# Kernel tuning notes

Measured on AMD Instinct MI355X. Metric: run time of the kernel, lower is better.

## Reference

```python
import jax, jax.numpy as jnp
import numpy as np

N, B, C, K, FF = 1024, 8, 256, 4, 2048

def layer_norm(x, g, b, eps=1e-5):
    mu = jnp.mean(x, axis=-1, keepdims=True)
    var = jnp.var(x, axis=-1, keepdims=True)
    return (x - mu) / jnp.sqrt(var + eps) * g + b

def setup_inputs() -> dict:
    key = jax.random.key(0)
    ks = jax.random.split(key, 10)
    s = 0.02
    return {
        "src_tokens": jax.random.normal(ks[0], (N, B, C), jnp.float32),
        "matched_token_list": jax.random.normal(ks[1], (K, N, B, C), jnp.float32),
        "pos_embed": jax.random.normal(ks[2], (N, B, C), jnp.float32),
        "mask": jnp.zeros((B, N, N), jnp.float32),
        "W_agg": jax.random.normal(ks[3], (C * K, C), jnp.float32) * s,
        "b_agg": jnp.zeros((C,), jnp.float32),
        "W1": jax.random.normal(ks[4], (C, FF), jnp.float32) * s,
        "b1": jnp.zeros((FF,), jnp.float32),
        "W2": jax.random.normal(ks[5], (FF, C), jnp.float32) * s,
        "b2": jnp.zeros((C,), jnp.float32),
        "g1": jnp.ones((C,), jnp.float32),
        "be1": jnp.zeros((C,), jnp.float32),
        "g2": jnp.ones((C,), jnp.float32),
        "be2": jnp.zeros((C,), jnp.float32),
    }

def reference(src_tokens, matched_token_list, pos_embed, mask,
              W_agg, b_agg, W1, b1, W2, b2, g1, be1, g2, be2):
    # q: (n,b,c) -> (b,n,c); k/v: (K,n,b,c) -> (K,b,n,c)
    q = jnp.transpose(src_tokens + pos_embed, (1, 0, 2))
    k = jnp.transpose(matched_token_list + pos_embed[None], (0, 2, 1, 3))
    v = jnp.transpose(matched_token_list, (0, 2, 1, 3))
    q_scaled = q / jnp.sqrt(jnp.asarray(q.shape[-1], q.dtype))
    # scores: (K,b,n,n) with additive mask bias
    scores = jnp.einsum('bnc,kbmc->kbnm', q_scaled, k) + mask[None]
    attn = jax.nn.softmax(scores, axis=-1)
    out_k = jnp.einsum('kbnm,kbmc->kbnc', attn, v)  # (K,b,n,c)
    # concat over K on channel dim: (b,n,K*c)
    cat = jnp.transpose(out_k, (1, 2, 0, 3)).reshape(q.shape[0], q.shape[1], -1)
    rec = cat @ W_agg + b_agg  # (b,n,c)
    rec = jnp.transpose(rec, (1, 0, 2))  # (n,b,c)
    rec = layer_norm(src_tokens + rec, g1, be1)
    ffn = jax.nn.relu(rec @ W1 + b1) @ W2 + b2
    rec = layer_norm(rec + ffn, g2, be2)
    return rec
```

## Files before the change

### kernel.cpp

```cpp
#include <hip/hip_runtime.h>

#define N_SEQ 1024
#define B_SZ 8
#define C_DIM 256
#define K_HEADS 4
#define FF_DIM 2048

typedef short s16x8 __attribute__((ext_vector_type(8)));
typedef float f32x4v __attribute__((ext_vector_type(4)));

#define GLOAD_LDS16(src, dst)                                                              \
    __builtin_amdgcn_global_load_lds((const __attribute__((address_space(1))) void*)(src), \
                                     (__attribute__((address_space(3))) void*)(dst), 16, 0, 0)

__device__ __forceinline__ unsigned short f2bf(float f) {
    unsigned u = __builtin_bit_cast(unsigned, f);
    u += 0x7FFFu + ((u >> 16) & 1u);
    return (unsigned short)(u >> 16);
}


__global__ __launch_bounds__(256) void prep_q_kernel(const float* __restrict__ src,
                                                     const float* __restrict__ pos,
                                                     unsigned short* __restrict__ qb) {
    int t = blockIdx.x * 256 + threadIdx.x;
    int i4 = t * 4;
    float4 s = *reinterpret_cast<const float4*>(src + i4);
    float4 p = *reinterpret_cast<const float4*>(pos + i4);
    int n = i4 >> 11;
    int rem = i4 & 2047;
    int b = rem >> 8;
    int c = rem & 255;
    int out = (b * N_SEQ + n) * C_DIM + c;
    *reinterpret_cast<ushort4*>(qb + out) = make_ushort4(
        f2bf((s.x + p.x) * 0.0625f), f2bf((s.y + p.y) * 0.0625f),
        f2bf((s.z + p.z) * 0.0625f), f2bf((s.w + p.w) * 0.0625f));
}

__global__ __launch_bounds__(256) void prep_kv_kernel(const float* __restrict__ matched,
                                                      const float* __restrict__ pos,
                                                      unsigned short* __restrict__ kb,
                                                      unsigned short* __restrict__ vfrag) {
    __shared__ unsigned short Vl[64][256];
    int blk = blockIdx.x;
    int nt = blk & 15, pr = blk >> 4;
    int k = pr >> 3, b = pr & 7;
    int n0 = nt * 64;
    int t = threadIdx.x;
    int c4 = (t & 63) * 4;
#pragma unroll
    for (int r = 0; r < 16; r++) {
        int nl = (t >> 6) * 16 + r;
        int n = n0 + nl;
        size_t mi = ((size_t)(k * N_SEQ + n) * B_SZ + b) * C_DIM + c4;
        float4 m = *reinterpret_cast<const float4*>(matched + mi);
        float4 p = *reinterpret_cast<const float4*>(pos + ((size_t)n * B_SZ + b) * C_DIM + c4);
        *reinterpret_cast<ushort4*>(kb + ((size_t)pr * N_SEQ + n) * C_DIM + c4) =
            make_ushort4(f2bf(m.x + p.x), f2bf(m.y + p.y), f2bf(m.z + p.z), f2bf(m.w + p.w));
        *reinterpret_cast<ushort4*>(&Vl[nl][c4]) =
            make_ushort4(f2bf(m.x), f2bf(m.y), f2bf(m.z), f2bf(m.w));
    }
    __syncthreads();
#pragma unroll
    for (int h = 0; h < 2; h++) {
        unsigned short* tb = vfrag + ((size_t)(pr * 32 + nt * 2 + h)) * 8192;
#pragma unroll
        for (int g = 0; g < 4; g++) {
            int c2 = t + 256 * g;
            int ct = c2 >> 6;
            int lane2 = c2 & 63;
            int l152 = lane2 & 15, lg2 = lane2 >> 4;
            s16x8 v;
#pragma unroll
            for (int e = 0; e < 8; e++)
                v[e] = (short)Vl[h * 32 + lg2 * 8 + e][ct * 16 + l152];
            *reinterpret_cast<s16x8*>(tb + (size_t)c2 * 8) = v;
        }
    }
}

__global__ __launch_bounds__(256) void transpose_w_kernel(const float* __restrict__ W,
                                                          unsigned short* __restrict__ Wt,
                                                          int R, int Cn) {
    int idx = blockIdx.x * 256 + threadIdx.x;
    int c = idx / R;
    int r = idx - c * R;
    Wt[idx] = f2bf(W[(size_t)r * Cn + c]);
}

__global__ __launch_bounds__(256, 2) void attn_kernel(const unsigned short* __restrict__ qb,
                                                      const unsigned short* __restrict__ kb,
                                                      const unsigned short* __restrict__ vfrag,
                                                      const float* __restrict__ mask,
                                                      unsigned short* __restrict__ att) {
    __shared__ unsigned short Kl[2][8192];
    __shared__ unsigned short Psh[2][4][16][40];
    __shared__ float scl[2][4][17];
    __shared__ float lrex[4][17];

    int bx = blockIdx.x;
    int b = bx & 7;
    int r2 = bx >> 3;
    int kidx = r2 & 3;
    int qtb = r2 >> 2;
    int pr = kidx * 8 + b;

    int tid = threadIdx.x, wid = tid >> 6, lane = tid & 63;
    int l15 = lane & 15, lg = lane >> 4;
    int q0 = qtb * 64 + wid * 16;

    s16x8 qf[8];
    const unsigned short* qrow = qb + ((size_t)(b * N_SEQ + q0 + l15)) * C_DIM + lg * 8;
#pragma unroll
    for (int cc = 0; cc < 8; cc++) qf[cc] = *reinterpret_cast<const s16x8*>(qrow + cc * 32);

    f32x4v oacc[16];
#pragma unroll
    for (int i = 0; i < 16; i++) oacc[i] = (f32x4v){0.f, 0.f, 0.f, 0.f};
    float mrun = -3e38f, lrun = 0.f;

    const unsigned short* kbp = kb + (size_t)pr * N_SEQ * C_DIM;
    const unsigned short* vfp = vfrag + (size_t)pr * 32 * 8192 + lane * 8;
    const float* mrow = mask + ((size_t)b * N_SEQ + q0 + l15) * N_SEQ;

    auto stage_k = [&](int kv0, unsigned short* buf) {
#pragma unroll
        for (int i = 0; i < 4; i++) {
            int ch = (wid * 4 + i) * 64 + lane;
            int r = ch >> 5;
            int ce = ((ch & 31) * 8) ^ ((r & 7) << 3);
            GLOAD_LDS16(kbp + (size_t)(kv0 + r) * C_DIM + ce, &buf[(wid * 4 + i) * 512]);
        }
    };

    stage_k(0, &Kl[0][0]);
    f32x4v mc0 = *reinterpret_cast<const f32x4v*>(mrow + lg * 4);
    f32x4v mc1 = *reinterpret_cast<const f32x4v*>(mrow + 16 + lg * 4);

    int swz = (l15 & 7) << 3;
    for (int t = 0; t < 32; t++) {
        int cur = t & 1;
        int kv0 = t * 32;
        __syncthreads();
        if (t + 1 < 32) stage_k(kv0 + 32, &Kl[cur ^ 1][0]);

        const unsigned short* vsrc = vfp + (size_t)t * 8192;
        s16x8 vreg[4];
#pragma unroll
        for (int c = 0; c < 4; c++)
            vreg[c] = *reinterpret_cast<const s16x8*>(vsrc + (wid * 4 + c) * 512);

        f32x4v s0 = {0.f, 0.f, 0.f, 0.f}, s1 = {0.f, 0.f, 0.f, 0.f};
        const unsigned short* KlB = &Kl[cur][0];
        __builtin_amdgcn_s_setprio(1);
#pragma unroll
        for (int cc = 0; cc < 8; cc++) {
            s16x8 k0 = *reinterpret_cast<const s16x8*>(KlB + l15 * 256 + ((cc * 32 + lg * 8) ^ swz));
            s16x8 k1 = *reinterpret_cast<const s16x8*>(KlB + (16 + l15) * 256 + ((cc * 32 + lg * 8) ^ swz));
            s0 = __builtin_amdgcn_mfma_f32_16x16x32_bf16(k0, qf[cc], s0, 0, 0, 0);
            s1 = __builtin_amdgcn_mfma_f32_16x16x32_bf16(k1, qf[cc], s1, 0, 0, 0);
        }
        __builtin_amdgcn_s_setprio(0);
#pragma unroll
        for (int jj = 0; jj < 4; jj++) { s0[jj] += mc0[jj]; s1[jj] += mc1[jj]; }
        if (t + 1 < 32) {
            mc0 = *reinterpret_cast<const f32x4v*>(mrow + kv0 + 32 + lg * 4);
            mc1 = *reinterpret_cast<const f32x4v*>(mrow + kv0 + 48 + lg * 4);
        }

        float pm = fmaxf(fmaxf(fmaxf(s0[0], s0[1]), fmaxf(s0[2], s0[3])),
                         fmaxf(fmaxf(s1[0], s1[1]), fmaxf(s1[2], s1[3])));
        pm = fmaxf(pm, __shfl_xor(pm, 16));
        pm = fmaxf(pm, __shfl_xor(pm, 32));
        float sc = 1.0f;
        if (__any(pm > mrun + 8.f)) {
            float mn = fmaxf(mrun, pm);
            sc = __expf(mrun - mn);
            mrun = mn;
        }
        float p0[4], p1[4];
#pragma unroll
        for (int jj = 0; jj < 4; jj++) {
            p0[jj] = __expf(s0[jj] - mrun);
            p1[jj] = __expf(s1[jj] - mrun);
        }
        float ps = (p0[0] + p0[1]) + (p0[2] + p0[3]) + (p1[0] + p1[1]) + (p1[2] + p1[3]);
        ps += __shfl_xor(ps, 16);
        ps += __shfl_xor(ps, 32);
        lrun = lrun * sc + ps;

        *reinterpret_cast<ushort4*>(&Psh[cur][wid][l15][lg * 4]) =
            make_ushort4(f2bf(p0[0]), f2bf(p0[1]), f2bf(p0[2]), f2bf(p0[3]));
        *reinterpret_cast<ushort4*>(&Psh[cur][wid][l15][16 + lg * 4]) =
            make_ushort4(f2bf(p1[0]), f2bf(p1[1]), f2bf(p1[2]), f2bf(p1[3]));
        if (lane < 16) scl[cur][wid][lane] = sc;
        __syncthreads();

        __builtin_amdgcn_s_setprio(1);
#pragma unroll
        for (int j = 0; j < 4; j++) {
            float scj = scl[cur][j][l15];
            s16x8 pf = *reinterpret_cast<const s16x8*>(&Psh[cur][j][l15][lg * 8]);
#pragma unroll
            for (int c = 0; c < 4; c++) {
                int idx = j * 4 + c;
#pragma unroll
                for (int jj = 0; jj < 4; jj++) oacc[idx][jj] *= scj;
                oacc[idx] = __builtin_amdgcn_mfma_f32_16x16x32_bf16(vreg[c], pf, oacc[idx], 0, 0, 0);
            }
        }
        __builtin_amdgcn_s_setprio(0);
    }

    if (lane < 16) lrex[wid][lane] = lrun;
    __syncthreads();
#pragma unroll
    for (int j = 0; j < 4; j++) {
        float invj = 1.0f / lrex[j][l15];
#pragma unroll
        for (int c = 0; c < 4; c++) {
            int idx = j * 4 + c;
            size_t orow = ((size_t)(b * N_SEQ + qtb * 64 + j * 16 + l15)) * (K_HEADS * C_DIM)
                          + kidx * C_DIM + wid * 64 + c * 16 + lg * 4;
            *reinterpret_cast<ushort4*>(att + orow) =
                make_ushort4(f2bf(oacc[idx][0] * invj), f2bf(oacc[idx][1] * invj),
                             f2bf(oacc[idx][2] * invj), f2bf(oacc[idx][3] * invj));
        }
    }
}

template <int BM, int BN, int RELU, int OUTBF>
__global__ __launch_bounds__(256) void gemm_bt_kernel(const unsigned short* __restrict__ A,
                                                      const unsigned short* __restrict__ Bt,
                                                      const float* __restrict__ bias,
                                                      float* __restrict__ Cf,
                                                      unsigned short* __restrict__ Cb,
                                                      int M, int Nn, int Kd) {
    constexpr int WAVES_N = (BM == 128) ? 2 : 4;
    constexpr int WN = BN / WAVES_N;
    constexpr int NT = WN / 16;
    constexpr int TILE = (BM + BN) * 64;
    constexpr int CALLS = (BM + BN) / 32;
    __shared__ unsigned short Sl[2][TILE];
    int tm0 = blockIdx.y * BM, tn0 = blockIdx.x * BN;
    int tid = threadIdx.x, wid = tid >> 6, lane = tid & 63;
    int l15 = lane & 15, lg = lane >> 4;
    int wm = (wid / WAVES_N) * 64, wn = (wid % WAVES_N) * WN;

    f32x4v acc[4][NT];
#pragma unroll
    for (int i = 0; i < 4; i++)
#pragma unroll
        for (int j = 0; j < NT; j++) acc[i][j] = (f32x4v){0.f, 0.f, 0.f, 0.f};

    auto stage = [&](int k0, unsigned short* buf) {
#pragma unroll
        for (int i = 0; i < CALLS; i++) {
            int chb = (i * 4 + wid) * 64;
            int ch = chb + lane;
            const unsigned short* src;
            if (chb < BM * 8) {
                int r = ch >> 3;
                int c8 = ((ch & 7) * 8) ^ ((r & 7) << 3);
                src = A + (size_t)(tm0 + r) * Kd + k0 + c8;
            } else {
                int ch2 = ch - BM * 8;
                int r = ch2 >> 3;
                int c8 = ((ch2 & 7) * 8) ^ ((r & 7) << 3);
                src = Bt + (size_t)(tn0 + r) * Kd + k0 + c8;
            }
            GLOAD_LDS16(src, buf + chb * 8);
        }
    };

    stage(0, &Sl[0][0]);
    int nk = Kd >> 6;
    int swz = (l15 & 7) << 3;
    for (int kt = 0; kt < nk; kt++) {
        int cur = kt & 1;
        __syncthreads();
        if (kt + 1 < nk) stage((kt + 1) * 64, &Sl[cur ^ 1][0]);
        const unsigned short* SA = &Sl[cur][0];
        const unsigned short* SB = SA + BM * 64;
        s16x8 af[4][2], bf[NT][2];
#pragma unroll
        for (int mt = 0; mt < 4; mt++)
#pragma unroll
            for (int h = 0; h < 2; h++)
                af[mt][h] = *reinterpret_cast<const s16x8*>(
                    SA + (wm + mt * 16 + l15) * 64 + ((h * 32 + lg * 8) ^ swz));
#pragma unroll
        for (int nt = 0; nt < NT; nt++)
#pragma unroll
            for (int h = 0; h < 2; h++)
                bf[nt][h] = *reinterpret_cast<const s16x8*>(
                    SB + (wn + nt * 16 + l15) * 64 + ((h * 32 + lg * 8) ^ swz));
        __builtin_amdgcn_s_setprio(1);
#pragma unroll
        for (int mt = 0; mt < 4; mt++)
#pragma unroll
            for (int nt = 0; nt < NT; nt++) {
                acc[mt][nt] = __builtin_amdgcn_mfma_f32_16x16x32_bf16(af[mt][0], bf[nt][0], acc[mt][nt], 0, 0, 0);
                acc[mt][nt] = __builtin_amdgcn_mfma_f32_16x16x32_bf16(af[mt][1], bf[nt][1], acc[mt][nt], 0, 0, 0);
            }
        __builtin_amdgcn_s_setprio(0);
    }

#pragma unroll
    for (int mt = 0; mt < 4; mt++) {
#pragma unroll
        for (int nt = 0; nt < NT; nt++) {
#pragma unroll
            for (int j = 0; j < 4; j++) {
                int row = tm0 + wm + mt * 16 + lg * 4 + j;
                int col = tn0 + wn + nt * 16 + l15;
                float v = acc[mt][nt][j] + bias[col];
                if (RELU) v = fmaxf(v, 0.f);
                if (OUTBF) Cb[(size_t)row * Nn + col] = f2bf(v);
                else       Cf[(size_t)row * Nn + col] = v;
            }
        }
    }
}

__global__ __launch_bounds__(256) void ln1_kernel(const float* __restrict__ src,
                                                  const float* __restrict__ recT,
                                                  const float* __restrict__ g,
                                                  const float* __restrict__ be,
                                                  float* __restrict__ outf,
                                                  unsigned short* __restrict__ outb) {
    int r = blockIdx.x * 4 + (threadIdx.x >> 6);
    int lane = threadIdx.x & 63;
    int n = r >> 3, b = r & 7;
    int c = lane * 4;
    float4 xs = *reinterpret_cast<const float4*>(src + (size_t)r * C_DIM + c);
    float4 xr = *reinterpret_cast<const float4*>(recT + ((size_t)(b * N_SEQ + n)) * C_DIM + c);
    float x[4] = {xs.x + xr.x, xs.y + xr.y, xs.z + xr.z, xs.w + xr.w};
    float s = x[0] + x[1] + x[2] + x[3];
    float q = x[0] * x[0] + x[1] * x[1] + x[2] * x[2] + x[3] * x[3];
#pragma unroll
    for (int d = 1; d < 64; d <<= 1) {
        s += __shfl_xor(s, d);
        q += __shfl_xor(q, d);
    }
    float mean = s * (1.f / 256.f);
    float var = q * (1.f / 256.f) - mean * mean;
    float rstd = rsqrtf(var + 1e-5f);
    float4 gv = *reinterpret_cast<const float4*>(g + c);
    float4 bv = *reinterpret_cast<const float4*>(be + c);
    float y0 = (x[0] - mean) * rstd * gv.x + bv.x;
    float y1 = (x[1] - mean) * rstd * gv.y + bv.y;
    float y2 = (x[2] - mean) * rstd * gv.z + bv.z;
    float y3 = (x[3] - mean) * rstd * gv.w + bv.w;
    *reinterpret_cast<float4*>(outf + (size_t)r * C_DIM + c) = make_float4(y0, y1, y2, y3);
    *reinterpret_cast<ushort4*>(outb + (size_t)r * C_DIM + c) =
        make_ushort4(f2bf(y0), f2bf(y1), f2bf(y2), f2bf(y3));
}

__global__ __launch_bounds__(256) void ln2_kernel(const float* __restrict__ rec1f,
                                                  const float* __restrict__ ffn,
                                                  const float* __restrict__ g,
                                                  const float* __restrict__ be,
                                                  float* __restrict__ out) {
    int r = blockIdx.x * 4 + (threadIdx.x >> 6);
    int lane = threadIdx.x & 63;
    int c = lane * 4;
    size_t base = (size_t)r * C_DIM + c;
    float4 xa = *reinterpret_cast<const float4*>(rec1f + base);
    float4 xb = *reinterpret_cast<const float4*>(ffn + base);
    float x[4] = {xa.x + xb.x, xa.y + xb.y, xa.z + xb.z, xa.w + xb.w};
    float s = x[0] + x[1] + x[2] + x[3];
    float q = x[0] * x[0] + x[1] * x[1] + x[2] * x[2] + x[3] * x[3];
#pragma unroll
    for (int d = 1; d < 64; d <<= 1) {
        s += __shfl_xor(s, d);
        q += __shfl_xor(q, d);
    }
    float mean = s * (1.f / 256.f);
    float var = q * (1.f / 256.f) - mean * mean;
    float rstd = rsqrtf(var + 1e-5f);
    float4 gv = *reinterpret_cast<const float4*>(g + c);
    float4 bv = *reinterpret_cast<const float4*>(be + c);
    *reinterpret_cast<float4*>(out + base) = make_float4(
        (x[0] - mean) * rstd * gv.x + bv.x,
        (x[1] - mean) * rstd * gv.y + bv.y,
        (x[2] - mean) * rstd * gv.z + bv.z,
        (x[3] - mean) * rstd * gv.w + bv.w);
}


extern "C" void kernel_launch(void* const* d_in, const int* in_sizes, int n_in,
                              void* d_out, int out_size, void* d_ws, size_t ws_size,
                              hipStream_t stream) {
    const float* src   = (const float*)d_in[0];
    const float* match = (const float*)d_in[1];
    const float* pos   = (const float*)d_in[2];
    const float* mask  = (const float*)d_in[3];
    const float* Wagg  = (const float*)d_in[4];
    const float* bagg  = (const float*)d_in[5];
    const float* W1    = (const float*)d_in[6];
    const float* b1    = (const float*)d_in[7];
    const float* W2    = (const float*)d_in[8];
    const float* b2    = (const float*)d_in[9];
    const float* g1    = (const float*)d_in[10];
    const float* be1   = (const float*)d_in[11];
    const float* g2    = (const float*)d_in[12];
    const float* be2   = (const float*)d_in[13];

    char* ws = (char*)d_ws;
    unsigned short* qb    = (unsigned short*)(ws + 0);
    unsigned short* kb    = (unsigned short*)(ws + 4194304);
    unsigned short* vfrag = (unsigned short*)(ws + 20971520);
    unsigned short* att   = (unsigned short*)(ws + 37748736);
    float*          rec_t = (float*)(ws + 57147392);
    float*          rec1f = (float*)(ws + 65536000);
    unsigned short* rec1b = (unsigned short*)(ws + 73924608);
    unsigned short* WaggT = (unsigned short*)(ws + 54525952);
    unsigned short* W1T   = (unsigned short*)(ws + 55050240);
    unsigned short* W2T   = (unsigned short*)(ws + 56098816);
    unsigned short* hid   = (unsigned short*)(ws + 4194304);
    float*          ffn   = (float*)(ws + 57147392);
    float* outp = (float*)d_out;

    prep_q_kernel<<<2048, 256, 0, stream>>>(src, pos, qb);
    prep_kv_kernel<<<512, 256, 0, stream>>>(match, pos, kb, vfrag);
    transpose_w_kernel<<<1024, 256, 0, stream>>>(Wagg, WaggT, K_HEADS * C_DIM, C_DIM);
    transpose_w_kernel<<<2048, 256, 0, stream>>>(W1, W1T, C_DIM, FF_DIM);
    transpose_w_kernel<<<2048, 256, 0, stream>>>(W2, W2T, FF_DIM, C_DIM);

    attn_kernel<<<512, 256, 0, stream>>>(qb, kb, vfrag, mask, att);

    gemm_bt_kernel<64, 128, 0, 0><<<dim3(2, 128), 256, 0, stream>>>(
        att, WaggT, bagg, rec_t, nullptr, B_SZ * N_SEQ, C_DIM, K_HEADS * C_DIM);
    ln1_kernel<<<2048, 256, 0, stream>>>(src, rec_t, g1, be1, rec1f, rec1b);
    gemm_bt_kernel<128, 128, 1, 1><<<dim3(16, 64), 256, 0, stream>>>(
        rec1b, W1T, b1, nullptr, hid, N_SEQ * B_SZ, FF_DIM, C_DIM);
    gemm_bt_kernel<64, 128, 0, 0><<<dim3(2, 128), 256, 0, stream>>>(
        hid, W2T, b2, ffn, nullptr, N_SEQ * B_SZ, C_DIM, FF_DIM);
    ln2_kernel<<<2048, 256, 0, stream>>>(rec1f, ffn, g2, be2, outp);
}
```

Before: 159.6 us.

## Split-K the narrow GEMMs, merge weight transposes, skip unit rescales in attention

```diff
diff --git a/kernel.cpp b/kernel.cpp
--- a/kernel.cpp
+++ b/kernel.cpp
@@ -17,6 +17,10 @@
     unsigned u = __builtin_bit_cast(unsigned, f);
     u += 0x7FFFu + ((u >> 16) & 1u);
     return (unsigned short)(u >> 16);
+}
+__device__ __forceinline__ float bf2f(unsigned short h) {
+    unsigned u = ((unsigned)h) << 16;
+    return __builtin_bit_cast(float, u);
 }
 
 
@@ -79,13 +83,25 @@
     }
 }
 
-__global__ __launch_bounds__(256) void transpose_w_kernel(const float* __restrict__ W,
-                                                          unsigned short* __restrict__ Wt,
-                                                          int R, int Cn) {
+__global__ __launch_bounds__(256) void transpose_all_kernel(const float* __restrict__ Wagg,
+                                                            const float* __restrict__ W1,
+                                                            const float* __restrict__ W2,
+                                                            unsigned short* __restrict__ WaggT,
+                                                            unsigned short* __restrict__ W1T,
+                                                            unsigned short* __restrict__ W2T) {
     int idx = blockIdx.x * 256 + threadIdx.x;
-    int c = idx / R;
-    int r = idx - c * R;
-    Wt[idx] = f2bf(W[(size_t)r * Cn + c]);
+    if (idx < 262144) {
+        int c = idx >> 10, r = idx & 1023;
+        WaggT[idx] = f2bf(Wagg[(size_t)r * 256 + c]);
+    } else if (idx < 786432) {
+        int i = idx - 262144;
+        int c = i >> 8, r = i & 255;
+        W1T[i] = f2bf(W1[(size_t)r * 2048 + c]);
+    } else {
+        int i = idx - 786432;
+        int c = i >> 11, r = i & 2047;
+        W2T[i] = f2bf(W2[(size_t)r * 256 + c]);
+    }
 }
 
 __global__ __launch_bounds__(256, 2) void attn_kernel(const unsigned short* __restrict__ qb,
@@ -201,11 +217,15 @@
         for (int j = 0; j < 4; j++) {
             float scj = scl[cur][j][l15];
             s16x8 pf = *reinterpret_cast<const s16x8*>(&Psh[cur][j][l15][lg * 8]);
+            if (__any(scj != 1.0f)) {
+#pragma unroll
+                for (int c = 0; c < 4; c++)
+#pragma unroll
+                    for (int jj = 0; jj < 4; jj++) oacc[j * 4 + c][jj] *= scj;
+            }
 #pragma unroll
             for (int c = 0; c < 4; c++) {
                 int idx = j * 4 + c;
-#pragma unroll
-                for (int jj = 0; jj < 4; jj++) oacc[idx][jj] *= scj;
                 oacc[idx] = __builtin_amdgcn_mfma_f32_16x16x32_bf16(vreg[c], pf, oacc[idx], 0, 0, 0);
             }
         }
@@ -229,11 +249,12 @@
     }
 }
 
-template <int BM, int BN, int RELU, int OUTBF>
+template <int BM, int BN, int RELU, int OUTBF, int SPLITK>
 __global__ __launch_bounds__(256) void gemm_bt_kernel(const unsigned short* __restrict__ A,
                                                       const unsigned short* __restrict__ Bt,
                                                       const float* __restrict__ bias,
-                                                      float* __restrict__ Cf,
+                                                      float* __restrict__ Cf0,
+                                                      float* __restrict__ Cf1,
                                                       unsigned short* __restrict__ Cb,
                                                       int M, int Nn, int Kd) {
     constexpr int WAVES_N = (BM == 128) ? 2 : 4;
@@ -243,6 +264,8 @@
     constexpr int CALLS = (BM + BN) / 32;
     __shared__ unsigned short Sl[2][TILE];
     int tm0 = blockIdx.y * BM, tn0 = blockIdx.x * BN;
+    int kz = (SPLITK == 2) ? blockIdx.z : 0;
+    int kbase = kz * (Kd / SPLITK);
     int tid = threadIdx.x, wid = tid >> 6, lane = tid & 63;
     int l15 = lane & 15, lg = lane >> 4;
     int wm = (wid / WAVES_N) * 64, wn = (wid % WAVES_N) * WN;
@@ -273,13 +296,13 @@
         }
     };
 
-    stage(0, &Sl[0][0]);
-    int nk = Kd >> 6;
+    stage(kbase, &Sl[0][0]);
+    int nk = (Kd / SPLITK) >> 6;
     int swz = (l15 & 7) << 3;
     for (int kt = 0; kt < nk; kt++) {
         int cur = kt & 1;
         __syncthreads();
-        if (kt + 1 < nk) stage((kt + 1) * 64, &Sl[cur ^ 1][0]);
+        if (kt + 1 < nk) stage(kbase + (kt + 1) * 64, &Sl[cur ^ 1][0]);
         const unsigned short* SA = &Sl[cur][0];
         const unsigned short* SB = SA + BM * 64;
         s16x8 af[4][2], bf[NT][2];
@@ -306,6 +329,7 @@
         __builtin_amdgcn_s_setprio(0);
     }
 
+    float* Cf = (SPLITK == 2 && kz) ? Cf1 : Cf0;
 #pragma unroll
     for (int mt = 0; mt < 4; mt++) {
 #pragma unroll
@@ -314,7 +338,8 @@
             for (int j = 0; j < 4; j++) {
                 int row = tm0 + wm + mt * 16 + lg * 4 + j;
                 int col = tn0 + wn + nt * 16 + l15;
-                float v = acc[mt][nt][j] + bias[col];
+                float bv = (SPLITK == 2 && kz) ? 0.f : bias[col];
+                float v = acc[mt][nt][j] + bv;
                 if (RELU) v = fmaxf(v, 0.f);
                 if (OUTBF) Cb[(size_t)row * Nn + col] = f2bf(v);
                 else       Cf[(size_t)row * Nn + col] = v;
@@ -324,18 +349,21 @@
 }
 
 __global__ __launch_bounds__(256) void ln1_kernel(const float* __restrict__ src,
-                                                  const float* __restrict__ recT,
+                                                  const float* __restrict__ p0,
+                                                  const float* __restrict__ p1,
                                                   const float* __restrict__ g,
                                                   const float* __restrict__ be,
-                                                  float* __restrict__ outf,
                                                   unsigned short* __restrict__ outb) {
     int r = blockIdx.x * 4 + (threadIdx.x >> 6);
     int lane = threadIdx.x & 63;
     int n = r >> 3, b = r & 7;
     int c = lane * 4;
+    size_t tb_ = ((size_t)(b * N_SEQ + n)) * C_DIM + c;
     float4 xs = *reinterpret_cast<const float4*>(src + (size_t)r * C_DIM + c);
-    float4 xr = *reinterpret_cast<const float4*>(recT + ((size_t)(b * N_SEQ + n)) * C_DIM + c);
-    float x[4] = {xs.x + xr.x, xs.y + xr.y, xs.z + xr.z, xs.w + xr.w};
+    float4 xa = *reinterpret_cast<const float4*>(p0 + tb_);
+    float4 xb = *reinterpret_cast<const float4*>(p1 + tb_);
+    float x[4] = {xs.x + xa.x + xb.x, xs.y + xa.y + xb.y,
+                  xs.z + xa.z + xb.z, xs.w + xa.w + xb.w};
     float s = x[0] + x[1] + x[2] + x[3];
     float q = x[0] * x[0] + x[1] * x[1] + x[2] * x[2] + x[3] * x[3];
 #pragma unroll
@@ -348,17 +376,14 @@
     float rstd = rsqrtf(var + 1e-5f);
     float4 gv = *reinterpret_cast<const float4*>(g + c);
     float4 bv = *reinterpret_cast<const float4*>(be + c);
-    float y0 = (x[0] - mean) * rstd * gv.x + bv.x;
-    float y1 = (x[1] - mean) * rstd * gv.y + bv.y;
-    float y2 = (x[2] - mean) * rstd * gv.z + bv.z;
-    float y3 = (x[3] - mean) * rstd * gv.w + bv.w;
-    *reinterpret_cast<float4*>(outf + (size_t)r * C_DIM + c) = make_float4(y0, y1, y2, y3);
-    *reinterpret_cast<ushort4*>(outb + (size_t)r * C_DIM + c) =
-        make_ushort4(f2bf(y0), f2bf(y1), f2bf(y2), f2bf(y3));
-}
-
-__global__ __launch_bounds__(256) void ln2_kernel(const float* __restrict__ rec1f,
-                                                  const float* __restrict__ ffn,
+    *reinterpret_cast<ushort4*>(outb + (size_t)r * C_DIM + c) = make_ushort4(
+        f2bf((x[0] - mean) * rstd * gv.x + bv.x), f2bf((x[1] - mean) * rstd * gv.y + bv.y),
+        f2bf((x[2] - mean) * rstd * gv.z + bv.z), f2bf((x[3] - mean) * rstd * gv.w + bv.w));
+}
+
+__global__ __launch_bounds__(256) void ln2_kernel(const unsigned short* __restrict__ rec1b,
+                                                  const float* __restrict__ p0,
+                                                  const float* __restrict__ p1,
                                                   const float* __restrict__ g,
                                                   const float* __restrict__ be,
                                                   float* __restrict__ out) {
@@ -366,9 +391,11 @@
     int lane = threadIdx.x & 63;
     int c = lane * 4;
     size_t base = (size_t)r * C_DIM + c;
-    float4 xa = *reinterpret_cast<const float4*>(rec1f + base);
-    float4 xb = *reinterpret_cast<const float4*>(ffn + base);
-    float x[4] = {xa.x + xb.x, xa.y + xb.y, xa.z + xb.z, xa.w + xb.w};
+    ushort4 xr = *reinterpret_cast<const ushort4*>(rec1b + base);
+    float4 xa = *reinterpret_cast<const float4*>(p0 + base);
+    float4 xb = *reinterpret_cast<const float4*>(p1 + base);
+    float x[4] = {bf2f(xr.x) + xa.x + xb.x, bf2f(xr.y) + xa.y + xb.y,
+                  bf2f(xr.z) + xa.z + xb.z, bf2f(xr.w) + xa.w + xb.w};
     float s = x[0] + x[1] + x[2] + x[3];
     float q = x[0] * x[0] + x[1] * x[1] + x[2] * x[2] + x[3] * x[3];
 #pragma unroll
@@ -412,30 +439,29 @@
     unsigned short* kb    = (unsigned short*)(ws + 4194304);
     unsigned short* vfrag = (unsigned short*)(ws + 20971520);
     unsigned short* att   = (unsigned short*)(ws + 37748736);
-    float*          rec_t = (float*)(ws + 57147392);
-    float*          rec1f = (float*)(ws + 65536000);
-    unsigned short* rec1b = (unsigned short*)(ws + 73924608);
     unsigned short* WaggT = (unsigned short*)(ws + 54525952);
     unsigned short* W1T   = (unsigned short*)(ws + 55050240);
     unsigned short* W2T   = (unsigned short*)(ws + 56098816);
+    float*          rec_p0 = (float*)(ws + 57147392);
+    float*          rec_p1 = (float*)(ws + 65536000);
+    unsigned short* rec1b = (unsigned short*)(ws + 0);
     unsigned short* hid   = (unsigned short*)(ws + 4194304);
-    float*          ffn   = (float*)(ws + 57147392);
+    float*          ffn_p0 = rec_p0;
+    float*          ffn_p1 = rec_p1;
     float* outp = (float*)d_out;
 
     prep_q_kernel<<<2048, 256, 0, stream>>>(src, pos, qb);
     prep_kv_kernel<<<512, 256, 0, stream>>>(match, pos, kb, vfrag);
-    transpose_w_kernel<<<1024, 256, 0, stream>>>(Wagg, WaggT, K_HEADS * C_DIM, C_DIM);
-    transpose_w_kernel<<<2048, 256, 0, stream>>>(W1, W1T, C_DIM, FF_DIM);
-    transpose_w_kernel<<<2048, 256, 0, stream>>>(W2, W2T, FF_DIM, C_DIM);
+    transpose_all_kernel<<<5120, 256, 0, stream>>>(Wagg, W1, W2, WaggT, W1T, W2T);
 
     attn_kernel<<<512, 256, 0, stream>>>(qb, kb, vfrag, mask, att);
 
-    gemm_bt_kernel<64, 128, 0, 0><<<dim3(2, 128), 256, 0, stream>>>(
-        att, WaggT, bagg, rec_t, nullptr, B_SZ * N_SEQ, C_DIM, K_HEADS * C_DIM);
-    ln1_kernel<<<2048, 256, 0, stream>>>(src, rec_t, g1, be1, rec1f, rec1b);
-    gemm_bt_kernel<128, 128, 1, 1><<<dim3(16, 64), 256, 0, stream>>>(
-        rec1b, W1T, b1, nullptr, hid, N_SEQ * B_SZ, FF_DIM, C_DIM);
-    gemm_bt_kernel<64, 128, 0, 0><<<dim3(2, 128), 256, 0, stream>>>(
-        hid, W2T, b2, ffn, nullptr, N_SEQ * B_SZ, C_DIM, FF_DIM);
-    ln2_kernel<<<2048, 256, 0, stream>>>(rec1f, ffn, g2, be2, outp);
-}
+    gemm_bt_kernel<64, 128, 0, 0, 2><<<dim3(2, 128, 2), 256, 0, stream>>>(
+        att, WaggT, bagg, rec_p0, rec_p1, nullptr, B_SZ * N_SEQ, C_DIM, K_HEADS * C_DIM);
+    ln1_kernel<<<2048, 256, 0, stream>>>(src, rec_p0, rec_p1, g1, be1, rec1b);
+    gemm_bt_kernel<128, 128, 1, 1, 1><<<dim3(16, 64), 256, 0, stream>>>(
+        rec1b, W1T, b1, nullptr, nullptr, hid, N_SEQ * B_SZ, FF_DIM, C_DIM);
+    gemm_bt_kernel<64, 128, 0, 0, 2><<<dim3(2, 128, 2), 256, 0, stream>>>(
+        hid, W2T, b2, ffn_p0, ffn_p1, nullptr, N_SEQ * B_SZ, C_DIM, FF_DIM);
+    ln2_kernel<<<2048, 256, 0, stream>>>(rec1b, ffn_p0, ffn_p1, g2, be2, outp);
+}
```

Result: faster. 145.1 us (-9.1%).
